# Kernel tuning notes

Measured on AMD Instinct MI355X. Metric: run time of the kernel, lower is better.

Reference implementation:

```python
import jax, jax.numpy as jnp
import numpy as np

B, H, L, D = 2, 16, 2048, 64


def setup_inputs() -> dict:
    key = jax.random.key(0)
    kq, kk, kv, km = jax.random.split(key, 4)
    q = jax.random.normal(kq, (B, H, L, D), dtype=jnp.float32)
    k = jax.random.normal(kk, (B, H, L, D), dtype=jnp.float32)
    v = jax.random.normal(kv, (B, H, L, D), dtype=jnp.float32)
    mask = jax.random.uniform(km, (B, L, L), dtype=jnp.float32)
    return {"q": q, "k": k, "v": v, "mask": mask}


def reference(q, k, v, mask):
    d_tensor = k.shape[-1]
    # score = q @ k^T / sqrt(d)  -> [B,H,L,L]
    score = jnp.einsum("bhqd,bhkd->bhqk", q, k) / jnp.sqrt(jnp.float32(d_tensor))
    # multiplicative mask, broadcast over heads (mask: [B,L,L] -> [B,1,L,L])
    score = score * mask[:, None, :, :]
    score = jax.nn.softmax(score, axis=-1)
    out = jnp.einsum("bhqk,bhkd->bhqd", score, v)
    return (out, score)
```

## Files before the change

### kernel.cpp

```cpp
#include <hip/hip_runtime.h>

typedef __attribute__((ext_vector_type(8))) short bf16x8;
typedef __attribute__((ext_vector_type(4))) float f32x4;
typedef __attribute__((ext_vector_type(4))) unsigned u32x4;

#define DEV static __device__ __forceinline__

constexpr int B_ = 2, H_ = 16, L_ = 2048, D_ = 64;
constexpr float SCALE = 0.125f;

DEV short f2bf(float f) {
  unsigned u = __builtin_bit_cast(unsigned, f);
  u += 0x7fffu + ((u >> 16) & 1u);
  return (short)(u >> 16);
}
DEV unsigned pk2(float lo, float hi) {
  return (unsigned)(unsigned short)f2bf(lo) | ((unsigned)(unsigned short)f2bf(hi) << 16);
}
DEV float bflo(unsigned u) { return __builtin_bit_cast(float, u << 16); }
DEV float bfhi(unsigned u) { return __builtin_bit_cast(float, u & 0xffff0000u); }

DEV bf16x8 frag_from(const float* src) {
  float4 f0 = *(const float4*)src;
  float4 f1 = *(const float4*)(src + 4);
  bf16x8 r;
  r[0] = f2bf(f0.x); r[1] = f2bf(f0.y); r[2] = f2bf(f0.z); r[3] = f2bf(f0.w);
  r[4] = f2bf(f1.x); r[5] = f2bf(f1.y); r[6] = f2bf(f1.z); r[7] = f2bf(f1.w);
  return r;
}

__global__ __launch_bounds__(256) void convert_k_kernel(
    const float* __restrict__ Kg, short* __restrict__ Kp) {
  const int tid = threadIdx.x;
  const int lane = tid & 63, half = (tid >> 6) & 1, sub = tid >> 7;
  const int blk = blockIdx.x;
  const int bh = blk >> 6;
  const int ktile = (((blk & 63) << 1) | sub);
  const int g = lane >> 4, ln = lane & 15;
  const float* src = Kg + ((size_t)bh * L_ + ktile * 16 + ln) * D_ + half * 32 + g * 8;
  bf16x8 f = frag_from(src);
  *(bf16x8*)(Kp + ((((size_t)(bh * 128 + ktile)) * 2 + half) * 64 + lane) * 8) = f;
}

__global__ __launch_bounds__(256) void convert_vt_kernel(
    const float* __restrict__ Vg, short* __restrict__ Vt) {
  const int tid = threadIdx.x;
  const int d = tid & 63, s = tid >> 6;
  const int bh = blockIdx.x >> 3, kc = blockIdx.x & 7;
  const float* src = Vg + (size_t)bh * L_ * D_ + (size_t)(kc * 256 + s * 64) * D_ + d;
  short* dst = Vt + (size_t)bh * D_ * L_ + (size_t)d * L_ + kc * 256 + s * 64;
#pragma unroll
  for (int i0 = 0; i0 < 8; ++i0) {
    bf16x8 r;
#pragma unroll
    for (int i = 0; i < 8; ++i) r[i] = f2bf(src[(i0 * 8 + i) * D_]);
    *(bf16x8*)(dst + i0 * 8) = r;
  }
}

DEV void stage_pre(short* dst, const short* vtsrc, int c, int tid) {
  const int d = tid >> 3, ks = tid & 7;
  const short* src = vtsrc + (size_t)d * L_ + c * 256 + ks * 32;
  bf16x8 v0 = *(const bf16x8*)(src + 0);
  bf16x8 v1 = *(const bf16x8*)(src + 8);
  bf16x8 v2 = *(const bf16x8*)(src + 16);
  bf16x8 v3 = *(const bf16x8*)(src + 24);
  char* row = (char*)dst + d * 512;
  const int swz = (d & 7) << 4;
  *(bf16x8*)(row + ((ks * 64 + 0) ^ swz)) = v0;
  *(bf16x8*)(row + ((ks * 64 + 16) ^ swz)) = v1;
  *(bf16x8*)(row + ((ks * 64 + 32) ^ swz)) = v2;
  *(bf16x8*)(row + ((ks * 64 + 48) ^ swz)) = v3;
}
DEV void stage_f32(short* dst, const float* vsrc, int c, int tid) {
  const int kp_ = tid & 127, dh = (tid >> 7) * 16;
  const float* r0 = vsrc + (size_t)(c * 256 + kp_ * 2) * D_ + dh;
  const float* r1 = r0 + D_;
  char* base = (char*)dst;
#pragma unroll
  for (int i = 0; i < 4; ++i) {
    float4 a = *(const float4*)(r0 + i * 4);
    float4 b = *(const float4*)(r1 + i * 4);
    unsigned p0 = pk2(a.x, b.x), p1 = pk2(a.y, b.y), p2 = pk2(a.z, b.z), p3 = pk2(a.w, b.w);
    const int dd = dh + i * 4;
    *(unsigned*)(base + (dd + 0) * 512 + ((kp_ * 4) ^ (((dd + 0) & 7) << 4))) = p0;
    *(unsigned*)(base + (dd + 1) * 512 + ((kp_ * 4) ^ (((dd + 1) & 7) << 4))) = p1;
    *(unsigned*)(base + (dd + 2) * 512 + ((kp_ * 4) ^ (((dd + 2) & 7) << 4))) = p2;
    *(unsigned*)(base + (dd + 3) * 512 + ((kp_ * 4) ^ (((dd + 3) & 7) << 4))) = p3;
  }
}

template <bool USEPRE>
__global__ __launch_bounds__(512, 4) void attn_fused(
    const float* __restrict__ Qg, const float* __restrict__ Kg,
    const short* __restrict__ Kp, const float* __restrict__ Vg,
    const short* __restrict__ Vtg, const float* __restrict__ Mg,
    float* __restrict__ Pg, float* __restrict__ Og) {
  const int tid = threadIdx.x;
  const int w = tid >> 6, lane = tid & 63;
  const int g = lane >> 4, ln = lane & 15;

  const int bid = blockIdx.x;
  const int wg = (bid & 7) * 512 + (bid >> 3);
  const int q0 = (wg & 127) << 4;
  const int bh = wg >> 7;
  const int b = bh >> 4;

  __shared__ short vt[2][64 * 256];
  __shared__ float red[8][16];

  const float* qp = Qg + (size_t)bh * L_ * D_;
  const float* mrow = Mg + (size_t)b * L_ * L_ + (size_t)(q0 + ln) * L_;
  float* prow = Pg + (size_t)bh * L_ * L_ + (size_t)(q0 + ln) * L_;

  bf16x8 qf0 = frag_from(qp + (size_t)(q0 + ln) * D_ + g * 8);
  bf16x8 qf1 = frag_from(qp + (size_t)(q0 + ln) * D_ + 32 + g * 8);

  unsigned pkv[32];
  float mx = -1e30f;
  const bf16x8* kpb = (const bf16x8*)Kp + ((size_t)bh * 128 + w) * 128 + lane;

#pragma unroll
  for (int j = 0; j < 16; ++j) {
    bf16x8 k0, k1;
    if (USEPRE) {
      k0 = kpb[j * 1024];
      k1 = kpb[j * 1024 + 64];
    } else {
      const float* kr = Kg + (size_t)bh * L_ * D_ + (size_t)((w + 8 * j) * 16 + ln) * D_;
      k0 = frag_from(kr + g * 8);
      k1 = frag_from(kr + 32 + g * 8);
    }
    f32x4 acc{0.f, 0.f, 0.f, 0.f};
    acc = __builtin_amdgcn_mfma_f32_16x16x32_bf16(k0, qf0, acc, 0, 0, 0);
    acc = __builtin_amdgcn_mfma_f32_16x16x32_bf16(k1, qf1, acc, 0, 0, 0);
    float4 mk = *(const float4*)(mrow + (w + 8 * j) * 16 + g * 4);
    float l0 = acc[0] * SCALE * mk.x;
    float l1 = acc[1] * SCALE * mk.y;
    float l2 = acc[2] * SCALE * mk.z;
    float l3 = acc[3] * SCALE * mk.w;
    mx = fmaxf(mx, fmaxf(fmaxf(l0, l1), fmaxf(l2, l3)));
    pkv[2 * j] = pk2(l0, l1);
    pkv[2 * j + 1] = pk2(l2, l3);
  }

  if (USEPRE) stage_pre(vt[0], Vtg + (size_t)bh * D_ * L_, 0, tid);
  else stage_f32(vt[0], Vg + (size_t)bh * L_ * D_, 0, tid);

  mx = fmaxf(mx, __shfl_xor(mx, 16));
  mx = fmaxf(mx, __shfl_xor(mx, 32));
  if (lane < 16) red[w][ln] = mx;
  __syncthreads();
  {
    float t = red[0][ln];
#pragma unroll
    for (int ww = 1; ww < 8; ++ww) t = fmaxf(t, red[ww][ln]);
    mx = t;
  }
  float sm = 0.f;
#pragma unroll
  for (int j = 0; j < 16; ++j) {
    float e0 = __expf(bflo(pkv[2 * j]) - mx);
    float e1 = __expf(bfhi(pkv[2 * j]) - mx);
    float e2 = __expf(bflo(pkv[2 * j + 1]) - mx);
    float e3 = __expf(bfhi(pkv[2 * j + 1]) - mx);
    sm += (e0 + e1) + (e2 + e3);
    pkv[2 * j] = pk2(e0, e1);
    pkv[2 * j + 1] = pk2(e2, e3);
  }
  sm += __shfl_xor(sm, 16);
  sm += __shfl_xor(sm, 32);
  __syncthreads();
  if (lane < 16) red[w][ln] = sm;
  __syncthreads();
  float inv;
  {
    float t = red[0][ln];
#pragma unroll
    for (int ww = 1; ww < 8; ++ww) t += red[ww][ln];
    inv = 1.0f / t;
  }

#pragma unroll
  for (int j = 0; j < 16; ++j) {
    float n0 = bflo(pkv[2 * j]) * inv, n1 = bfhi(pkv[2 * j]) * inv;
    float n2 = bflo(pkv[2 * j + 1]) * inv, n3 = bfhi(pkv[2 * j + 1]) * inv;
    f32x4 st{n0, n1, n2, n3};
    __builtin_nontemporal_store(st, (f32x4*)(prow + (w + 8 * j) * 16 + g * 4));
    pkv[2 * j] = pk2(n0, n1);
    pkv[2 * j + 1] = pk2(n2, n3);
  }

  f32x4 acc_o[4];
#pragma unroll
  for (int n = 0; n < 4; ++n) acc_o[n] = f32x4{0.f, 0.f, 0.f, 0.f};

  const short* vsrc_pre = Vtg + (size_t)bh * D_ * L_;
  const float* vsrc_f32 = Vg + (size_t)bh * L_ * D_;
  const int boff = w * 32 + g * 8;

#pragma unroll
  for (int c = 0; c < 8; ++c) {
    if (c < 7) {
      if (USEPRE) stage_pre(vt[(c + 1) & 1], vsrc_pre, c + 1, tid);
      else stage_f32(vt[(c + 1) & 1], vsrc_f32, c + 1, tid);
    }
    u32x4 au{pkv[4 * c], pkv[4 * c + 1], pkv[4 * c + 2], pkv[4 * c + 3]};
    bf16x8 pa = __builtin_bit_cast(bf16x8, au);
    const char* buf = (const char*)vt[c & 1];
#pragma unroll
    for (int n = 0; n < 4; ++n) {
      const int d = n * 16 + ln;
      const char* rowp = buf + d * 512;
      const int off = boff ^ ((d & 7) << 4);
      uint2 lo = *(const uint2*)(rowp + off);
      uint2 hi = *(const uint2*)(rowp + off + 256);
      u32x4 bu{lo.x, lo.y, hi.x, hi.y};
      acc_o[n] = __builtin_amdgcn_mfma_f32_16x16x32_bf16(
          pa, __builtin_bit_cast(bf16x8, bu), acc_o[n], 0, 0, 0);
    }
    __syncthreads();
  }

  float* red_o = (float*)vt;
#pragma unroll
  for (int n = 0; n < 4; ++n)
#pragma unroll
    for (int r = 0; r < 4; ++r)
      red_o[(w * 16 + g * 4 + r) * 64 + n * 16 + ln] = acc_o[n][r];
  __syncthreads();
  {
    float* ob = Og + (size_t)bh * L_ * D_ + (size_t)q0 * D_;
    const int row = tid >> 5, dp = (tid & 31) * 2;
    float s0 = 0.f, s1 = 0.f;
#pragma unroll
    for (int ww = 0; ww < 8; ++ww) {
      s0 += red_o[(ww * 16 + row) * 64 + dp];
      s1 += red_o[(ww * 16 + row) * 64 + dp + 1];
    }
    __builtin_nontemporal_store(s0, ob + row * D_ + dp);
    __builtin_nontemporal_store(s1, ob + row * D_ + dp + 1);
  }
}

extern "C" void kernel_launch(void* const* d_in, const int* in_sizes, int n_in,
                              void* d_out, int out_size, void* d_ws, size_t ws_size,
                              hipStream_t stream) {
  const float* q = (const float*)d_in[0];
  const float* k = (const float*)d_in[1];
  const float* v = (const float*)d_in[2];
  const float* mask = (const float*)d_in[3];
  float* out = (float*)d_out;
  float* score = out + (size_t)B_ * H_ * L_ * D_;

  const size_t elems = (size_t)B_ * H_ * L_ * D_;
  const size_t need = elems * 2 * sizeof(short);
  const int nblk = B_ * H_ * (L_ / 16);

  if (ws_size >= need) {
    short* kp = (short*)d_ws;
    short* vtg = kp + elems;
    convert_k_kernel<<<2048, 256, 0, stream>>>(k, kp);
    convert_vt_kernel<<<B_ * H_ * 8, 256, 0, stream>>>(v, vtg);
    attn_fused<true><<<nblk, 512, 0, stream>>>(q, k, kp, v, vtg, mask, score, out);
  } else {
    attn_fused<false><<<nblk, 512, 0, stream>>>(q, k, nullptr, v, nullptr, mask, score, out);
  }
}
```

Before: 270.9 us.

## Prepack V into MFMA fragment layout and read directly from global memory

The V conversion kernel now writes V in the exact per-lane bf16 MFMA B-fragment order, going through shared memory to transpose. The fused attention kernel then loads each V fragment straight from global or L2 and drops the double-buffered LDS staging of V and the per-chunk barriers. This removes the LDS traffic and synchronisation from the PV loop, at the cost of uncached global fragment loads. The launch-bounds occupancy hint drops from 4 to 2 blocks per CU, and the fallback path now does scattered scalar global loads.

```diff
diff --git a/kernel.cpp b/kernel.cpp
--- a/kernel.cpp
+++ b/kernel.cpp
@@ -42,59 +42,48 @@
   *(bf16x8*)(Kp + ((((size_t)(bh * 128 + ktile)) * 2 + half) * 64 + lane) * 8) = f;
 }
 
-__global__ __launch_bounds__(256) void convert_vt_kernel(
-    const float* __restrict__ Vg, short* __restrict__ Vt) {
+__global__ __launch_bounds__(256) void convert_vp_kernel(
+    const float* __restrict__ Vg, short* __restrict__ Vp) {
+  __shared__ short vt[64 * 256];
   const int tid = threadIdx.x;
-  const int d = tid & 63, s = tid >> 6;
-  const int bh = blockIdx.x >> 3, kc = blockIdx.x & 7;
-  const float* src = Vg + (size_t)bh * L_ * D_ + (size_t)(kc * 256 + s * 64) * D_ + d;
-  short* dst = Vt + (size_t)bh * D_ * L_ + (size_t)d * L_ + kc * 256 + s * 64;
-#pragma unroll
-  for (int i0 = 0; i0 < 8; ++i0) {
-    bf16x8 r;
-#pragma unroll
-    for (int i = 0; i < 8; ++i) r[i] = f2bf(src[(i0 * 8 + i) * D_]);
-    *(bf16x8*)(dst + i0 * 8) = r;
-  }
-}
-
-DEV void stage_pre(short* dst, const short* vtsrc, int c, int tid) {
-  const int d = tid >> 3, ks = tid & 7;
-  const short* src = vtsrc + (size_t)d * L_ + c * 256 + ks * 32;
-  bf16x8 v0 = *(const bf16x8*)(src + 0);
-  bf16x8 v1 = *(const bf16x8*)(src + 8);
-  bf16x8 v2 = *(const bf16x8*)(src + 16);
-  bf16x8 v3 = *(const bf16x8*)(src + 24);
-  char* row = (char*)dst + d * 512;
-  const int swz = (d & 7) << 4;
-  *(bf16x8*)(row + ((ks * 64 + 0) ^ swz)) = v0;
-  *(bf16x8*)(row + ((ks * 64 + 16) ^ swz)) = v1;
-  *(bf16x8*)(row + ((ks * 64 + 32) ^ swz)) = v2;
-  *(bf16x8*)(row + ((ks * 64 + 48) ^ swz)) = v3;
-}
-DEV void stage_f32(short* dst, const float* vsrc, int c, int tid) {
-  const int kp_ = tid & 127, dh = (tid >> 7) * 16;
-  const float* r0 = vsrc + (size_t)(c * 256 + kp_ * 2) * D_ + dh;
+  const int bh = blockIdx.x >> 3, c = blockIdx.x & 7;
+  const float* vb = Vg + (size_t)bh * L_ * D_ + (size_t)c * 256 * D_;
+  const int ka = (tid & 127) * 2, dh = (tid >> 7) * 32;
+  const float* r0 = vb + (size_t)ka * D_ + dh;
   const float* r1 = r0 + D_;
-  char* base = (char*)dst;
-#pragma unroll
-  for (int i = 0; i < 4; ++i) {
+#pragma unroll
+  for (int i = 0; i < 8; ++i) {
     float4 a = *(const float4*)(r0 + i * 4);
     float4 b = *(const float4*)(r1 + i * 4);
     unsigned p0 = pk2(a.x, b.x), p1 = pk2(a.y, b.y), p2 = pk2(a.z, b.z), p3 = pk2(a.w, b.w);
     const int dd = dh + i * 4;
-    *(unsigned*)(base + (dd + 0) * 512 + ((kp_ * 4) ^ (((dd + 0) & 7) << 4))) = p0;
-    *(unsigned*)(base + (dd + 1) * 512 + ((kp_ * 4) ^ (((dd + 1) & 7) << 4))) = p1;
-    *(unsigned*)(base + (dd + 2) * 512 + ((kp_ * 4) ^ (((dd + 2) & 7) << 4))) = p2;
-    *(unsigned*)(base + (dd + 3) * 512 + ((kp_ * 4) ^ (((dd + 3) & 7) << 4))) = p3;
+    *(unsigned*)((char*)vt + (dd + 0) * 512 + ((ka * 2) ^ (((dd + 0) & 7) << 4))) = p0;
+    *(unsigned*)((char*)vt + (dd + 1) * 512 + ((ka * 2) ^ (((dd + 1) & 7) << 4))) = p1;
+    *(unsigned*)((char*)vt + (dd + 2) * 512 + ((ka * 2) ^ (((dd + 2) & 7) << 4))) = p2;
+    *(unsigned*)((char*)vt + (dd + 3) * 512 + ((ka * 2) ^ (((dd + 3) & 7) << 4))) = p3;
+  }
+  __syncthreads();
+  u32x4* out = (u32x4*)Vp + (size_t)(bh * 8 + c) * 2048;
+#pragma unroll
+  for (int i = 0; i < 8; ++i) {
+    const int u = tid + 256 * i;
+    const int lane = u & 63, w = (u >> 6) & 7, n = u >> 9;
+    const int g = lane >> 4, ln = lane & 15;
+    const int d = n * 16 + ln;
+    const int kb = (w * 16 + g * 4) * 2;
+    const char* rowp = (const char*)vt + d * 512;
+    const int swz = (d & 7) << 4;
+    uint2 lo = *(const uint2*)(rowp + (kb ^ swz));
+    uint2 hi = *(const uint2*)(rowp + ((kb + 256) ^ swz));
+    out[u] = u32x4{lo.x, lo.y, hi.x, hi.y};
   }
 }
 
 template <bool USEPRE>
-__global__ __launch_bounds__(512, 4) void attn_fused(
+__global__ __launch_bounds__(512, 2) void attn_fused(
     const float* __restrict__ Qg, const float* __restrict__ Kg,
     const short* __restrict__ Kp, const float* __restrict__ Vg,
-    const short* __restrict__ Vtg, const float* __restrict__ Mg,
+    const short* __restrict__ Vpg, const float* __restrict__ Mg,
     float* __restrict__ Pg, float* __restrict__ Og) {
   const int tid = threadIdx.x;
   const int w = tid >> 6, lane = tid & 63;
@@ -106,7 +95,7 @@
   const int bh = wg >> 7;
   const int b = bh >> 4;
 
-  __shared__ short vt[2][64 * 256];
+  __shared__ float red_o[128 * 64];
   __shared__ float red[8][16];
 
   const float* qp = Qg + (size_t)bh * L_ * D_;
@@ -144,9 +133,6 @@
     pkv[2 * j + 1] = pk2(l2, l3);
   }
 
-  if (USEPRE) stage_pre(vt[0], Vtg + (size_t)bh * D_ * L_, 0, tid);
-  else stage_f32(vt[0], Vg + (size_t)bh * L_ * D_, 0, tid);
-
   mx = fmaxf(mx, __shfl_xor(mx, 16));
   mx = fmaxf(mx, __shfl_xor(mx, 32));
   if (lane < 16) red[w][ln] = mx;
@@ -195,34 +181,30 @@
 #pragma unroll
   for (int n = 0; n < 4; ++n) acc_o[n] = f32x4{0.f, 0.f, 0.f, 0.f};
 
-  const short* vsrc_pre = Vtg + (size_t)bh * D_ * L_;
-  const float* vsrc_f32 = Vg + (size_t)bh * L_ * D_;
-  const int boff = w * 32 + g * 8;
+  const u32x4* vp4 = (const u32x4*)Vpg + (size_t)bh * 8 * 2048;
 
 #pragma unroll
   for (int c = 0; c < 8; ++c) {
-    if (c < 7) {
-      if (USEPRE) stage_pre(vt[(c + 1) & 1], vsrc_pre, c + 1, tid);
-      else stage_f32(vt[(c + 1) & 1], vsrc_f32, c + 1, tid);
-    }
     u32x4 au{pkv[4 * c], pkv[4 * c + 1], pkv[4 * c + 2], pkv[4 * c + 3]};
     bf16x8 pa = __builtin_bit_cast(bf16x8, au);
-    const char* buf = (const char*)vt[c & 1];
 #pragma unroll
     for (int n = 0; n < 4; ++n) {
-      const int d = n * 16 + ln;
-      const char* rowp = buf + d * 512;
-      const int off = boff ^ ((d & 7) << 4);
-      uint2 lo = *(const uint2*)(rowp + off);
-      uint2 hi = *(const uint2*)(rowp + off + 256);
-      u32x4 bu{lo.x, lo.y, hi.x, hi.y};
-      acc_o[n] = __builtin_amdgcn_mfma_f32_16x16x32_bf16(
-          pa, __builtin_bit_cast(bf16x8, bu), acc_o[n], 0, 0, 0);
+      bf16x8 bf;
+      if (USEPRE) {
+        bf = __builtin_bit_cast(bf16x8, vp4[(size_t)c * 2048 + (n * 8 + w) * 64 + lane]);
+      } else {
+        const int d = n * 16 + ln;
+        const int k0 = c * 256 + w * 16 + g * 4;
+        const float* vb = Vg + (size_t)bh * L_ * D_ + d;
+#pragma unroll
+        for (int e = 0; e < 4; ++e) bf[e] = f2bf(vb[(size_t)(k0 + e) * D_]);
+#pragma unroll
+        for (int e = 0; e < 4; ++e) bf[4 + e] = f2bf(vb[(size_t)(k0 + 128 + e) * D_]);
+      }
+      acc_o[n] = __builtin_amdgcn_mfma_f32_16x16x32_bf16(pa, bf, acc_o[n], 0, 0, 0);
     }
-    __syncthreads();
-  }
-
-  float* red_o = (float*)vt;
+  }
+
 #pragma unroll
   for (int n = 0; n < 4; ++n)
 #pragma unroll
@@ -259,10 +241,10 @@
 
   if (ws_size >= need) {
     short* kp = (short*)d_ws;
-    short* vtg = kp + elems;
+    short* vp = kp + elems;
     convert_k_kernel<<<2048, 256, 0, stream>>>(k, kp);
-    convert_vt_kernel<<<B_ * H_ * 8, 256, 0, stream>>>(v, vtg);
-    attn_fused<true><<<nblk, 512, 0, stream>>>(q, k, kp, v, vtg, mask, score, out);
+    convert_vp_kernel<<<B_ * H_ * 8, 256, 0, stream>>>(v, vp);
+    attn_fused<true><<<nblk, 512, 0, stream>>>(q, k, kp, v, vp, mask, score, out);
   } else {
     attn_fused<false><<<nblk, 512, 0, stream>>>(q, k, nullptr, v, nullptr, mask, score, out);
   }
```

New measurement: 288.5 us. +6.5%, slower.
